# Kernel optimization log

Hardware: AMD Instinct MI355X
Metric: run time of the kernel (lower is better)

Reference implementation:

```python
import jax, jax.numpy as jnp
import numpy as np

N, E, D, H = 50000, 800000, 128, 8
HD = D // H
EPS = 1e-5


def _layernorm(x, w, b):
    # Custom LayerNorm from the repo: divides by (unbiased std + eps), not sqrt(var+eps)
    mu = x.mean(axis=-1, keepdims=True)
    sd = x.std(axis=-1, keepdims=True, ddof=1)
    return (x - mu) / (sd + EPS) * w + b


def setup_inputs() -> dict:
    key = jax.random.key(0)
    ks = jax.random.split(key, 16)
    s = 1.0 / np.sqrt(D)
    inp = {
        "feats": jax.random.normal(ks[0], (N, D), jnp.float32),
        "edge_index": jax.random.randint(ks[1], (E, 2), 0, N, jnp.int32),
        "Wq": jax.random.normal(ks[2], (D, D), jnp.float32) * s,
        "bq": jnp.zeros((D,), jnp.float32),
        "Wk": jax.random.normal(ks[3], (D, D), jnp.float32) * s,
        "bk": jnp.zeros((D,), jnp.float32),
        "Wv": jax.random.normal(ks[4], (D, D), jnp.float32) * s,
        "bv": jnp.zeros((D,), jnp.float32),
        "Wo": jax.random.normal(ks[5], (D, D), jnp.float32) * s,
        "bo": jnp.zeros((D,), jnp.float32),
        "ln1_w": jnp.ones((D,), jnp.float32),
        "ln1_b": jnp.zeros((D,), jnp.float32),
        "ln2_w": jnp.ones((D,), jnp.float32),
        "ln2_b": jnp.zeros((D,), jnp.float32),
        "W1": jax.random.normal(ks[6], (4 * D, D), jnp.float32) * s,
        "b1": jnp.zeros((4 * D,), jnp.float32),
        "W2": jax.random.normal(ks[7], (D, 4 * D), jnp.float32) * (1.0 / np.sqrt(4 * D)),
        "b2": jnp.zeros((D,), jnp.float32),
    }
    return inp


def reference(feats, edge_index, Wq, bq, Wk, bk, Wv, bv, Wo, bo,
              ln1_w, ln1_b, ln2_w, ln2_b, W1, b1, W2, b2):
    n = feats.shape[0]
    row, col = edge_index[:, 0], edge_index[:, 1]

    # --- multi-head dot-product attention over edges (dropout = identity, eval mode) ---
    x2 = _layernorm(feats, ln1_w, ln1_b)
    q = (x2 @ Wq.T + bq).reshape(n, H, HD)
    k = (x2 @ Wk.T + bk).reshape(n, H, HD)
    v = (x2 @ Wv.T + bv).reshape(n, H, HD)

    # per-edge scores: q[col] . k[row] / sqrt(head_dim)  -> [E, H]
    scores = jnp.einsum('ehd,ehd->eh', q[col], k[row]) / np.sqrt(HD).astype(np.float32)

    # scatter softmax normalized over groups of `row`
    smax = jax.ops.segment_max(scores, row, num_segments=n)       # [N, H]
    ex = jnp.exp(scores - smax[row])                              # [E, H]
    denom = jax.ops.segment_sum(ex, row, num_segments=n)         # [N, H]
    alpha = ex / denom[row]                                       # [E, H]

    # weighted messages, aggregated at col via scatter_add
    msg = alpha[:, :, None] * v[row]                              # [E, H, HD]
    agg = jax.ops.segment_sum(msg, col, num_segments=n).reshape(n, D)
    att = agg @ Wo.T + bo

    feats = feats + att  # residual 1

    # --- MLP block: note ReLU after BOTH linears (fc_dims=[4D, D], D != 1) ---
    x2 = _layernorm(feats, ln2_w, ln2_b)
    h = jax.nn.relu(x2 @ W1.T + b1)
    h = jax.nn.relu(h @ W2.T + b2)
    feats = feats + h  # residual 2
    return feats
```

## Files before the change

kernel.cpp:

```cpp
#include <hip/hip_runtime.h>
#include <hip/hip_bf16.h>
#include <math.h>

#define H_HEADS 8
constexpr float LN_EPS = 1e-5f;
constexpr int NBCH = 64;
constexpr int NSEG = 4;

using short8 = __attribute__((ext_vector_type(8))) short;
using f32x4  = __attribute__((ext_vector_type(4))) float;
using half2v = __attribute__((ext_vector_type(2))) _Float16;

#if defined(__has_builtin)
#  if __has_builtin(__builtin_amdgcn_fdot2)
#    define HAS_FDOT2 1
#  endif
#endif
#ifndef HAS_FDOT2
#  define HAS_FDOT2 0
#endif

__device__ __forceinline__ ushort f2bf(float v){
  __hip_bfloat16 h = __float2bfloat16(v);
  return *reinterpret_cast<ushort*>(&h);
}
__device__ __forceinline__ float bf2f(ushort u){
  return __uint_as_float(((unsigned)u) << 16);
}

__device__ __forceinline__ void stage16(const ushort* g, ushort* l){
  __builtin_amdgcn_global_load_lds((const __attribute__((address_space(1))) unsigned*)g,
                                   (__attribute__((address_space(3))) unsigned*)l,
                                   16, 0, 0);
}

__global__ void ln_kernel(const float* __restrict__ x, const float* __restrict__ w,
                          const float* __restrict__ b, ushort* __restrict__ out, int nrows){
  int wid = threadIdx.x >> 6, lane = threadIdx.x & 63;
  int r = blockIdx.x * (blockDim.x >> 6) + wid;
  if (r >= nrows) return;
  float2 v = ((const float2*)(x + (size_t)r*128))[lane];
  float s = v.x + v.y;
  #pragma unroll
  for (int o = 32; o; o >>= 1) s += __shfl_xor(s, o);
  float mu = s * (1.0f/128.0f);
  float d0 = v.x - mu, d1 = v.y - mu;
  float ss = d0*d0 + d1*d1;
  #pragma unroll
  for (int o = 32; o; o >>= 1) ss += __shfl_xor(ss, o);
  float sd = sqrtf(ss * (1.0f/127.0f));
  float inv = 1.0f / (sd + LN_EPS);
  float2 wv = ((const float2*)w)[lane];
  float2 bv = ((const float2*)b)[lane];
  ushort2 o2 = { f2bf(d0*inv*wv.x + bv.x), f2bf(d1*inv*wv.y + bv.y) };
  ((ushort2*)(out + (size_t)r*128))[lane] = o2;
}

struct CvtArgs { const float* s[6]; ushort* d[6]; int cnt[6]; };
__global__ void cvt6_kernel(CvtArgs a){
  int w = blockIdx.y;
  int i = blockIdx.x*blockDim.x + threadIdx.x;
  if (i < a.cnt[w]) a.d[w][i] = f2bf(a.s[w][i]);
}

template<int K, int RELU, int RESID, int OUTMODE>
__device__ __forceinline__ void gemm_lds_body(
    const ushort* __restrict__ A, const ushort* __restrict__ W,
    const float* __restrict__ bias, const float* __restrict__ resid,
    void* __restrict__ out, int M, int Nout, int cb, ushort* Wl){
  constexpr int NCH = K / 128;
  int t = threadIdx.x;
  int wid = t >> 6, lane = t & 63;
  int mb = blockIdx.x * 64 + wid * 16;
  int lrow = lane & 15, kgrp = lane >> 4;
  int row = mb + lrow;
  bool rowok = row < M;
  const ushort* arow = A + (size_t)(rowok ? row : (M-1)) * K + kgrp*8;

  f32x4 acc[8] = {};
  short8 af[2][4];

  #pragma unroll
  for (int p = 0; p < 8; ++p){
    int L = p*256 + t;
    int colp = L >> 4, sp = L & 15;
    stage16(W + (size_t)colp*K + ((sp ^ (colp & 7)) << 3),
            (ushort*)((char*)Wl + ((size_t)(p*256 + (t & ~63)))*16));
  }
  #pragma unroll
  for (int kk = 0; kk < 4; ++kk)
    af[0][kk] = *(const short8*)(arow + kk*32);

  #pragma unroll
  for (int ci = 0; ci < NCH; ++ci){
    __syncthreads();
    int cur = ci & 1;
    if (ci + 1 < NCH){
      #pragma unroll
      for (int kk = 0; kk < 4; ++kk)
        af[cur^1][kk] = *(const short8*)(arow + (ci+1)*128 + kk*32);
    }
    #pragma unroll
    for (int kk = 0; kk < 4; ++kk){
      #pragma unroll
      for (int nt = 0; nt < 8; ++nt){
        int colc = nt*16 + lrow;
        int g = kk*4 + kgrp;
        short8 bfv = *(const short8*)((const char*)Wl + colc*256 + ((g ^ (colc & 7))*16));
        acc[nt] = __builtin_amdgcn_mfma_f32_16x16x32_bf16(af[cur][kk], bfv, acc[nt], 0, 0, 0);
      }
    }
    if (ci + 1 < NCH){
      __syncthreads();
      const ushort* Wc = W + (ci+1)*128;
      #pragma unroll
      for (int p = 0; p < 8; ++p){
        int L = p*256 + t;
        int colp = L >> 4, sp = L & 15;
        stage16(Wc + (size_t)colp*K + ((sp ^ (colp & 7)) << 3),
                (ushort*)((char*)Wl + ((size_t)(p*256 + (t & ~63)))*16));
      }
    }
  }

  int r0 = mb + kgrp*4;
  #pragma unroll
  for (int nt = 0; nt < 8; ++nt){
    int c = cb + nt*16 + lrow;
    float bsum = bias[c];
    #pragma unroll
    for (int i = 0; i < 4; ++i){
      int r = r0 + i;
      if (r >= M) continue;
      float v = acc[nt][i] + bsum;
      if (RELU)  v = fmaxf(v, 0.0f);
      if (RESID) v += resid[(size_t)r*Nout + c];
      if (OUTMODE == 1) ((ushort*)out)[(size_t)r*Nout + c] = f2bf(v);
      else if (OUTMODE == 2){
        _Float16 hv = (_Float16)v;
        ((ushort*)out)[(size_t)r*Nout + c] = __builtin_bit_cast(ushort, hv);
      } else ((float*)out)[(size_t)r*Nout + c] = v;
    }
  }
}

template<int K, int RELU, int RESID, int OUTMODE>
__global__ __launch_bounds__(256) void gemm_lds(
    const ushort* __restrict__ A, const ushort* __restrict__ Wfull,
    const float* __restrict__ bias, const float* __restrict__ resid,
    void* __restrict__ out, int M, int Nout){
  __shared__ __align__(16) ushort Wl[16384];
  int cb = blockIdx.y * 128;
  gemm_lds_body<K,RELU,RESID,OUTMODE>(A, Wfull + (size_t)cb*K, bias, resid, out, M, Nout, cb, Wl);
}

__global__ __launch_bounds__(256) void qkv_lds(
    const ushort* __restrict__ A, const ushort* __restrict__ Wcat,
    const float* __restrict__ bq, const float* __restrict__ bk, const float* __restrict__ bv,
    ushort* __restrict__ qb, ushort* __restrict__ kb, ushort* __restrict__ vb, int M){
  __shared__ __align__(16) ushort Wl[16384];
  int y = blockIdx.y;
  const float* bias = (y==0) ? bq : (y==1) ? bk : bv;
  ushort* out = (y==0) ? qb : (y==1) ? kb : vb;
  if (y == 2)
    gemm_lds_body<128,0,0,1>(A, Wcat + (size_t)y*16384, bias, nullptr, out, M, 128, 0, Wl);
  else
    gemm_lds_body<128,0,0,2>(A, Wcat + (size_t)y*16384, bias, nullptr, out, M, 128, 0, Wl);
}

__global__ __launch_bounds__(256) void hist_seg2(const int* __restrict__ ei,
    unsigned* __restrict__ copies, int E, int n, int nw, int chunk, int nsb){
  __shared__ unsigned hh[12544];
  int b = blockIdx.x, s = blockIdx.y, t = threadIdx.x;
  int bin0 = s * nsb;
  int bin1 = min(bin0 + nsb, n);
  int words = (bin1 - bin0 + 1) >> 1;
  for (int i = t; i < 2*words; i += 256) hh[i] = 0;
  __syncthreads();
  int lo = b*chunk, hi = min(lo + chunk, E);
  for (int e = lo + t; e < hi; e += 256){
    int2 rc = ((const int2*)ei)[e];
    if (rc.x >= bin0 && rc.x < bin1)
      atomicAdd(&hh[(rc.x - bin0) >> 1], 1u << ((rc.x & 1)*16));
    if (rc.y >= bin0 && rc.y < bin1)
      atomicAdd(&hh[words + ((rc.y - bin0) >> 1)], 1u << ((rc.y & 1)*16));
  }
  __syncthreads();
  unsigned* d0 = copies + (size_t)b*nw + (bin0 >> 1);
  unsigned* d1 = copies + (size_t)(NBCH + b)*nw + (bin0 >> 1);
  for (int i = t; i < words; i += 256){ d0[i] = hh[i]; d1[i] = hh[words + i]; }
}

__global__ __launch_bounds__(256) void scan_fold(const unsigned* __restrict__ copies,
    int* __restrict__ cnt2, ushort* __restrict__ choff, int n, int nw){
  int y = blockIdx.y;
  int bin = blockIdx.x*256 + threadIdx.x;
  if (bin >= n) return;
  const unsigned* cp = copies + (size_t)y*NBCH*nw + (bin >> 1);
  int sh = (bin & 1)*16;
  int run = 0;
  for (int b = 0; b < NBCH; ++b){
    int c = (int)((cp[(size_t)b*nw] >> sh) & 0xffffu);
    choff[((size_t)y*NBCH + b)*n + bin] = (ushort)run;
    run += c;
  }
  cnt2[(size_t)y*n + bin] = run;
}

__global__ __launch_bounds__(256) void scan_reduce(const int* __restrict__ cnt0,
                                                   int* __restrict__ partial, int n, int nb){
  const int* cnt = cnt0 + (size_t)blockIdx.y * n;
  int t = threadIdx.x;
  int base = blockIdx.x*1024 + t*4;
  int s = 0;
  #pragma unroll
  for (int j = 0; j < 4; ++j){ int i = base+j; if (i < n) s += cnt[i]; }
  __shared__ int sm[256];
  sm[t] = s; __syncthreads();
  for (int off = 128; off; off >>= 1){
    if (t < off) sm[t] += sm[t+off];
    __syncthreads();
  }
  if (t == 0) partial[blockIdx.y*nb + blockIdx.x] = sm[0];
}

__global__ __launch_bounds__(256) void scan_mid(int* __restrict__ partial, int nb,
                                                int* __restrict__ rptr, int* __restrict__ cptr, int n){
  int y = blockIdx.y;
  int* p = partial + y*nb;
  int t = threadIdx.x;
  __shared__ int sm[256];
  sm[t] = (t < nb) ? p[t] : 0;
  __syncthreads();
  for (int off = 1; off < 256; off <<= 1){
    int v = (t >= off) ? sm[t-off] : 0;
    __syncthreads();
    sm[t] += v;
    __syncthreads();
  }
  if (t < nb) p[t] = (t == 0) ? 0 : sm[t-1];
  if (t == 0) (y ? cptr : rptr)[n] = sm[255];
}

__global__ __launch_bounds__(256) void scan_scatter(const int* __restrict__ cnt0,
                                                    const int* __restrict__ partial,
                                                    int* __restrict__ rptr, int* __restrict__ cptr,
                                                    int n, int nb){
  int y = blockIdx.y;
  const int* cnt = cnt0 + (size_t)y * n;
  int* ptr = y ? cptr : rptr;
  int t = threadIdx.x;
  int base = blockIdx.x*1024 + t*4;
  int v[4]; int s = 0;
  #pragma unroll
  for (int j = 0; j < 4; ++j){ int i = base+j; v[j] = (i<n)?cnt[i]:0; s += v[j]; }
  __shared__ int sm[256];
  sm[t] = s; __syncthreads();
  for (int off = 1; off < 256; off <<= 1){
    int x = (t >= off) ? sm[t-off] : 0;
    __syncthreads();
    sm[t] += x;
    __syncthreads();
  }
  int pre = partial[y*nb + blockIdx.x] + ((t==0)?0:sm[t-1]);
  #pragma unroll
  for (int j = 0; j < 4; ++j){
    int i = base+j;
    if (i < n){ ptr[i] = pre; pre += v[j]; }
  }
}

__global__ __launch_bounds__(256) void fill_r_seg(const int* __restrict__ ei,
    const int* __restrict__ rptr, const ushort* __restrict__ choffR,
    int* __restrict__ rcol, int* __restrict__ pose, int E, int n, int chunk, int nsb){
  __shared__ unsigned hh[8192];
  int b = blockIdx.x, s = blockIdx.y, t = threadIdx.x;
  int bin0 = s * nsb;
  int bin1 = min(bin0 + nsb, n);
  int words = (bin1 - bin0 + 1) >> 1;
  for (int i = t; i < words; i += 256) hh[i] = 0;
  __syncthreads();
  const ushort* chb = choffR + (size_t)b*n;
  int lo = b*chunk, hi = min(lo + chunk, E);
  for (int e = lo + t; e < hi; e += 256){
    int2 rc = ((const int2*)ei)[e];
    int bin = rc.x;
    if (bin < bin0 || bin >= bin1) continue;
    int sh = (bin & 1)*16;
    unsigned old = atomicAdd(&hh[(bin - bin0) >> 1], 1u << sh);
    int rank = (int)((old >> sh) & 0xffffu);
    int pos = rptr[bin] + (int)chb[bin] + rank;
    rcol[pos] = rc.y;
    pose[e] = pos;
  }
}

__global__ __launch_bounds__(256) void fill_c_seg(const int* __restrict__ ei,
    const int* __restrict__ cptr, const ushort* __restrict__ choffC,
    const int* __restrict__ pose, int* __restrict__ crow, int* __restrict__ cposr,
    int E, int n, int chunk, int nsb){
  __shared__ unsigned hh[8192];
  int b = blockIdx.x, s = blockIdx.y, t = threadIdx.x;
  int bin0 = s * nsb;
  int bin1 = min(bin0 + nsb, n);
  int words = (bin1 - bin0 + 1) >> 1;
  for (int i = t; i < words; i += 256) hh[i] = 0;
  __syncthreads();
  const ushort* chb = choffC + (size_t)b*n;
  int lo = b*chunk, hi = min(lo + chunk, E);
  for (int e = lo + t; e < hi; e += 256){
    int2 rc = ((const int2*)ei)[e];
    int bin = rc.y;
    if (bin < bin0 || bin >= bin1) continue;
    int sh = (bin & 1)*16;
    unsigned old = atomicAdd(&hh[(bin - bin0) >> 1], 1u << sh);
    int rank = (int)((old >> sh) & 0xffffu);
    int pos = cptr[bin] + (int)chb[bin] + rank;
    crow[pos] = rc.x;
    cposr[pose[e]] = pos;
  }
}

__device__ __forceinline__ float qdot16h(const ushort* __restrict__ qb, int c, int h,
                                         const half2v* kf2){
  const int4* qp = (const int4*)(qb + (size_t)c*128 + h*16);
  int4 a = qp[0], b = qp[1];
  int qa[8] = {a.x, a.y, a.z, a.w, b.x, b.y, b.z, b.w};
  float s = 0.f;
#if HAS_FDOT2
  #pragma unroll
  for (int i = 0; i < 8; ++i)
    s = __builtin_amdgcn_fdot2(__builtin_bit_cast(half2v, qa[i]), kf2[i], s, false);
#else
  #pragma unroll
  for (int i = 0; i < 8; ++i){
    half2v q2 = __builtin_bit_cast(half2v, qa[i]);
    s += (float)q2.x * (float)kf2[i].x + (float)q2.y * (float)kf2[i].y;
  }
#endif
  return s * 0.25f;
}

template<int NS>
__device__ __forceinline__ void softmax_rows(const ushort* __restrict__ qb,
    const int* __restrict__ rcol, const int* __restrict__ cposr,
    ushort* __restrict__ cbuf, const half2v* kf2, int lo, int hi, int h, int el){
  float sreg[NS];
  float m = -1e30f;
  #pragma unroll
  for (int ts = 0; ts < NS; ++ts){
    int j = lo + el + ts*8;
    float s = (j < hi) ? qdot16h(qb, rcol[j], h, kf2) : -1e30f;
    sreg[ts] = s;
    m = fmaxf(m, s);
  }
  if (NS == 8)
    for (int j = lo + el + 64; j < hi; j += 8)
      m = fmaxf(m, qdot16h(qb, rcol[j], h, kf2));
  #pragma unroll
  for (int o = 8; o < 64; o <<= 1) m = fmaxf(m, __shfl_xor(m, o));

  float d = 0.f;
  #pragma unroll
  for (int ts = 0; ts < NS; ++ts){
    int j = lo + el + ts*8;
    if (j < hi){ float e = __expf(sreg[ts] - m); sreg[ts] = e; d += e; }
  }
  if (NS == 8)
    for (int j = lo + el + 64; j < hi; j += 8)
      d += __expf(qdot16h(qb, rcol[j], h, kf2) - m);
  #pragma unroll
  for (int o = 8; o < 64; o <<= 1) d += __shfl_xor(d, o);
  float invd = 1.0f / d;

  #pragma unroll
  for (int ts = 0; ts < NS; ++ts){
    int j = lo + el + ts*8;
    if (j < hi) cbuf[(size_t)cposr[j]*8 + h] = f2bf(sreg[ts] * invd);
  }
  if (NS == 8)
    for (int j = lo + el + 64; j < hi; j += 8){
      float s = qdot16h(qb, rcol[j], h, kf2);
      cbuf[(size_t)cposr[j]*8 + h] = f2bf(__expf(s - m) * invd);
    }
}

__global__ void row_softmax_kernel(const ushort* __restrict__ qb, const ushort* __restrict__ kb,
                                   const int* __restrict__ rptr, const int* __restrict__ rcol,
                                   const int* __restrict__ cposr,
                                   ushort* __restrict__ cbuf, int n){
  int wid = threadIdx.x >> 6, lane = threadIdx.x & 63;
  int r = blockIdx.x * (blockDim.x >> 6) + wid;
  if (r >= n) return;
  int lo = rptr[r], hi = rptr[r+1];
  if (lo >= hi) return;
  int h = lane & 7, el = lane >> 3;

  half2v kf2[8];
  {
    const int4* kp = (const int4*)(kb + (size_t)r*128 + h*16);
    int4 k0 = kp[0], k1 = kp[1];
    kf2[0] = __builtin_bit_cast(half2v, k0.x);
    kf2[1] = __builtin_bit_cast(half2v, k0.y);
    kf2[2] = __builtin_bit_cast(half2v, k0.z);
    kf2[3] = __builtin_bit_cast(half2v, k0.w);
    kf2[4] = __builtin_bit_cast(half2v, k1.x);
    kf2[5] = __builtin_bit_cast(half2v, k1.y);
    kf2[6] = __builtin_bit_cast(half2v, k1.z);
    kf2[7] = __builtin_bit_cast(half2v, k1.w);
  }

  int deg = hi - lo;
  if (deg <= 16)      softmax_rows<2>(qb, rcol, cposr, cbuf, kf2, lo, hi, h, el);
  else if (deg <= 32) softmax_rows<4>(qb, rcol, cposr, cbuf, kf2, lo, hi, h, el);
  else                softmax_rows<8>(qb, rcol, cposr, cbuf, kf2, lo, hi, h, el);
}

__global__ void agg_kernel(const ushort* __restrict__ vb, const ushort* __restrict__ cbuf,
                           const int* __restrict__ cptr, const int* __restrict__ crow,
                           ushort* __restrict__ aggb, int n){
  int wid = threadIdx.x >> 6, lane = threadIdx.x & 63;
  int node = blockIdx.x * (blockDim.x >> 6) + wid;
  if (node >= n) return;
  int lo = cptr[node], hi = cptr[node+1];
  int oct = lane >> 3, l8 = lane & 7;
  float acc[16] = {};
  for (int j = lo + oct; j < hi; j += 8){
    float a = bf2f(cbuf[(size_t)j*8 + l8]);
    int row = crow[j];
    const short8* vp = (const short8*)(vb + (size_t)row*128 + l8*16);
    short8 v0 = vp[0], v1 = vp[1];
    #pragma unroll
    for (int i = 0; i < 8; ++i){
      acc[i]   = fmaf(a, bf2f((ushort)v0[i]), acc[i]);
      acc[8+i] = fmaf(a, bf2f((ushort)v1[i]), acc[8+i]);
    }
  }
  #pragma unroll
  for (int i = 0; i < 16; ++i){
    acc[i] += __shfl_xor(acc[i], 8);
    acc[i] += __shfl_xor(acc[i], 16);
    acc[i] += __shfl_xor(acc[i], 32);
  }
  if (oct == 0){
    short8 o0, o1;
    #pragma unroll
    for (int i = 0; i < 8; ++i){ o0[i] = (short)f2bf(acc[i]); o1[i] = (short)f2bf(acc[8+i]); }
    short8* op = (short8*)(aggb + (size_t)node*128 + l8*16);
    op[0] = o0; op[1] = o1;
  }
}

extern "C" void kernel_launch(void* const* d_in, const int* in_sizes, int n_in,
                              void* d_out, int out_size, void* d_ws, size_t ws_size,
                              hipStream_t stream){
  const float* feats = (const float*)d_in[0];
  const int*   ei    = (const int*)  d_in[1];
  const float* Wq = (const float*)d_in[2];
  const float* bq = (const float*)d_in[3];
  const float* Wk = (const float*)d_in[4];
  const float* bk = (const float*)d_in[5];
  const float* Wv = (const float*)d_in[6];
  const float* bv = (const float*)d_in[7];
  const float* Wo = (const float*)d_in[8];
  const float* bo = (const float*)d_in[9];
  const float* ln1w = (const float*)d_in[10];
  const float* ln1b = (const float*)d_in[11];
  const float* ln2w = (const float*)d_in[12];
  const float* ln2b = (const float*)d_in[13];
  const float* W1 = (const float*)d_in[14];
  const float* b1 = (const float*)d_in[15];
  const float* W2 = (const float*)d_in[16];
  const float* b2 = (const float*)d_in[17];
  float* outp = (float*)d_out;

  int n = in_sizes[0] / 128;
  int E = in_sizes[1] / 2;
  int nw = (n + 1) >> 1;
  int chunk = (E + NBCH - 1) / NBCH;
  int nsb = (((n + NSEG - 1) / NSEG) + 1) & ~1;

  const size_t ND  = (size_t)n * 128;
  const size_t ND2 = ND / 2;
  const size_t EH  = (size_t)E * H_HEADS;

  float* ws = (float*)d_ws;
  ushort* x2b  = (ushort*)ws;
  ushort* qb   = (ushort*)(ws + ND2);
  ushort* kb   = (ushort*)(ws + 2*ND2);
  ushort* vb   = (ushort*)(ws + 3*ND2);
  ushort* cbuf = (ushort*)(ws + 4*ND2);
  ushort* aggb = (ushort*)(ws + 4*ND2 + EH/2);
  int* crow    = (int*)(ws + 5*ND2 + EH/2);
  int* cposr   = crow + E;
  int* rcol    = cposr + E;
  int* pose    = rcol + E;
  int* rptr    = pose + E;
  int* cptr    = rptr + (n + 4);
  int* cnt2    = cptr + (n + 4);
  ushort* choff = (ushort*)(cnt2 + 2*n);
  unsigned* copies = (unsigned*)(choff + (size_t)2*NBCH*n);
  int* partial = (int*)(copies + (size_t)2*NBCH*nw);
  ushort* wbuf = (ushort*)(partial + 512);
  ushort* Wqb = wbuf;
  ushort* Wkb = Wqb + 16384;
  ushort* Wvb = Wkb + 16384;
  ushort* Wob = Wvb + 16384;
  ushort* W1b = Wob + 16384;
  ushort* W2b = W1b + 65536;
  ushort* h1  = qb;

  CvtArgs ca;
  ca.s[0]=Wq; ca.s[1]=Wk; ca.s[2]=Wv; ca.s[3]=Wo; ca.s[4]=W1; ca.s[5]=W2;
  ca.d[0]=Wqb; ca.d[1]=Wkb; ca.d[2]=Wvb; ca.d[3]=Wob; ca.d[4]=W1b; ca.d[5]=W2b;
  ca.cnt[0]=ca.cnt[1]=ca.cnt[2]=ca.cnt[3]=16384; ca.cnt[4]=ca.cnt[5]=65536;
  cvt6_kernel<<<dim3(65536/256, 6), 256, 0, stream>>>(ca);

  int nb = (n + 1023)/1024;
  hist_seg2 <<<dim3(NBCH,NSEG), 256, 0, stream>>>(ei, copies, E, n, nw, chunk, nsb);
  scan_fold <<<dim3((n+255)/256,2), 256, 0, stream>>>(copies, cnt2, choff, n, nw);
  scan_reduce <<<dim3(nb,2), 256, 0, stream>>>(cnt2, partial, n, nb);
  scan_mid    <<<dim3(1,2),  256, 0, stream>>>(partial, nb, rptr, cptr, n);
  scan_scatter<<<dim3(nb,2), 256, 0, stream>>>(cnt2, partial, rptr, cptr, n, nb);
  fill_r_seg<<<dim3(NBCH,NSEG), 256, 0, stream>>>(ei, rptr, choff,                  rcol, pose, E, n, chunk, nsb);
  fill_c_seg<<<dim3(NBCH,NSEG), 256, 0, stream>>>(ei, cptr, choff + (size_t)NBCH*n, pose, crow, cposr, E, n, chunk, nsb);

  ln_kernel<<<(n+3)/4, 256, 0, stream>>>(feats, ln1w, ln1b, x2b, n);

  int gm = (n + 63)/64;
  qkv_lds<<<dim3(gm,3), 256, 0, stream>>>(x2b, Wqb, bq, bk, bv, qb, kb, vb, n);

  row_softmax_kernel<<<(n+3)/4, 256, 0, stream>>>(qb, kb, rptr, rcol, cposr, cbuf, n);

  agg_kernel<<<(n+3)/4, 256, 0, stream>>>(vb, cbuf, cptr, crow, aggb, n);

  gemm_lds<128,0,1,0><<<dim3(gm,1), 256, 0, stream>>>(aggb, Wob, bo, feats, outp, n, 128);

  ln_kernel<<<(n+3)/4, 256, 0, stream>>>(outp, ln2w, ln2b, x2b, n);

  gemm_lds<128,1,0,1><<<dim3(gm,4), 256, 0, stream>>>(x2b, W1b, b1, nullptr, h1,  n, 512);
  gemm_lds<512,1,1,0><<<dim3(gm,1), 256, 0, stream>>>(h1,  W2b, b2, outp,    outp, n, 128);
}
```

Measured before the change: 305.2 us.

## Fuse Wo GEMM with residual and LayerNorm2; use 128-row 512-thread GEMM blocks

Adds a gemm_wo_ln2 kernel that computes the output projection, adds bias and the residual, then applies LayerNorm2 in registers and writes the bf16 x2b buffer directly. This removes the separate ln_kernel launch and one fp32 read of outp. All GEMM blocks now cover 128 rows with 512 threads, so each block stages the weight tile once for twice as many rows. Waves past M skip loads and compute but still reach the barriers. The larger blocks mean fewer blocks in total and possibly lower occupancy.

```diff
diff --git a/kernel.cpp b/kernel.cpp
--- a/kernel.cpp
+++ b/kernel.cpp
@@ -71,9 +71,10 @@
   constexpr int NCH = K / 128;
   int t = threadIdx.x;
   int wid = t >> 6, lane = t & 63;
-  int mb = blockIdx.x * 64 + wid * 16;
+  int mb = blockIdx.x * 128 + wid * 16;
   int lrow = lane & 15, kgrp = lane >> 4;
   int row = mb + lrow;
+  bool waveok = mb < M;
   bool rowok = row < M;
   const ushort* arow = A + (size_t)(rowok ? row : (M-1)) * K + kgrp*8;
 
@@ -81,47 +82,52 @@
   short8 af[2][4];
 
   #pragma unroll
-  for (int p = 0; p < 8; ++p){
-    int L = p*256 + t;
+  for (int p = 0; p < 4; ++p){
+    int L = p*512 + t;
     int colp = L >> 4, sp = L & 15;
     stage16(W + (size_t)colp*K + ((sp ^ (colp & 7)) << 3),
-            (ushort*)((char*)Wl + ((size_t)(p*256 + (t & ~63)))*16));
-  }
-  #pragma unroll
-  for (int kk = 0; kk < 4; ++kk)
-    af[0][kk] = *(const short8*)(arow + kk*32);
+            (ushort*)((char*)Wl + ((size_t)(p*512 + (t & ~63)))*16));
+  }
+  if (waveok){
+    #pragma unroll
+    for (int kk = 0; kk < 4; ++kk)
+      af[0][kk] = *(const short8*)(arow + kk*32);
+  }
 
   #pragma unroll
   for (int ci = 0; ci < NCH; ++ci){
     __syncthreads();
     int cur = ci & 1;
-    if (ci + 1 < NCH){
+    if (waveok){
+      if (ci + 1 < NCH){
+        #pragma unroll
+        for (int kk = 0; kk < 4; ++kk)
+          af[cur^1][kk] = *(const short8*)(arow + (ci+1)*128 + kk*32);
+      }
       #pragma unroll
-      for (int kk = 0; kk < 4; ++kk)
-        af[cur^1][kk] = *(const short8*)(arow + (ci+1)*128 + kk*32);
-    }
-    #pragma unroll
-    for (int kk = 0; kk < 4; ++kk){
-      #pragma unroll
-      for (int nt = 0; nt < 8; ++nt){
-        int colc = nt*16 + lrow;
-        int g = kk*4 + kgrp;
-        short8 bfv = *(const short8*)((const char*)Wl + colc*256 + ((g ^ (colc & 7))*16));
-        acc[nt] = __builtin_amdgcn_mfma_f32_16x16x32_bf16(af[cur][kk], bfv, acc[nt], 0, 0, 0);
+      for (int kk = 0; kk < 4; ++kk){
+        #pragma unroll
+        for (int nt = 0; nt < 8; ++nt){
+          int colc = nt*16 + lrow;
+          int g = kk*4 + kgrp;
+          short8 bfv = *(const short8*)((const char*)Wl + colc*256 + ((g ^ (colc & 7))*16));
+          acc[nt] = __builtin_amdgcn_mfma_f32_16x16x32_bf16(af[cur][kk], bfv, acc[nt], 0, 0, 0);
+        }
       }
     }
     if (ci + 1 < NCH){
       __syncthreads();
       const ushort* Wc = W + (ci+1)*128;
       #pragma unroll
-      for (int p = 0; p < 8; ++p){
-        int L = p*256 + t;
+      for (int p = 0; p < 4; ++p){
+        int L = p*512 + t;
         int colp = L >> 4, sp = L & 15;
         stage16(Wc + (size_t)colp*K + ((sp ^ (colp & 7)) << 3),
-                (ushort*)((char*)Wl + ((size_t)(p*256 + (t & ~63)))*16));
+                (ushort*)((char*)Wl + ((size_t)(p*512 + (t & ~63)))*16));
       }
     }
   }
+  if (!waveok) return;
 
   int r0 = mb + kgrp*4;
   #pragma unroll
@@ -145,7 +151,7 @@
 }
 
 template<int K, int RELU, int RESID, int OUTMODE>
-__global__ __launch_bounds__(256) void gemm_lds(
+__global__ __launch_bounds__(512) void gemm_lds(
     const ushort* __restrict__ A, const ushort* __restrict__ Wfull,
     const float* __restrict__ bias, const float* __restrict__ resid,
     void* __restrict__ out, int M, int Nout){
@@ -154,7 +160,7 @@
   gemm_lds_body<K,RELU,RESID,OUTMODE>(A, Wfull + (size_t)cb*K, bias, resid, out, M, Nout, cb, Wl);
 }
 
-__global__ __launch_bounds__(256) void qkv_lds(
+__global__ __launch_bounds__(512) void qkv_lds(
     const ushort* __restrict__ A, const ushort* __restrict__ Wcat,
     const float* __restrict__ bq, const float* __restrict__ bk, const float* __restrict__ bv,
     ushort* __restrict__ qb, ushort* __restrict__ kb, ushort* __restrict__ vb, int M){
@@ -166,6 +172,97 @@
     gemm_lds_body<128,0,0,1>(A, Wcat + (size_t)y*16384, bias, nullptr, out, M, 128, 0, Wl);
   else
     gemm_lds_body<128,0,0,2>(A, Wcat + (size_t)y*16384, bias, nullptr, out, M, 128, 0, Wl);
+}
+
+__global__ __launch_bounds__(512) void gemm_wo_ln2(
+    const ushort* __restrict__ A, const ushort* __restrict__ W,
+    const float* __restrict__ bias, const float* __restrict__ feats,
+    const float* __restrict__ lnw, const float* __restrict__ lnb,
+    float* __restrict__ outp, ushort* __restrict__ x2b, int M){
+  constexpr int K = 128;
+  __shared__ __align__(16) ushort Wl[16384];
+  int t = threadIdx.x;
+  int wid = t >> 6, lane = t & 63;
+  int mb = blockIdx.x * 128 + wid * 16;
+  int lrow = lane & 15, kgrp = lane >> 4;
+  int row = mb + lrow;
+  bool waveok = mb < M;
+  bool rowok = row < M;
+  const ushort* arow = A + (size_t)(rowok ? row : (M-1)) * K + kgrp*8;
+
+  f32x4 acc[8] = {};
+  short8 af[4];
+
+  #pragma unroll
+  for (int p = 0; p < 4; ++p){
+    int L = p*512 + t;
+    int colp = L >> 4, sp = L & 15;
+    stage16(W + (size_t)colp*K + ((sp ^ (colp & 7)) << 3),
+            (ushort*)((char*)Wl + ((size_t)(p*512 + (t & ~63)))*16));
+  }
+  if (waveok){
+    #pragma unroll
+    for (int kk = 0; kk < 4; ++kk)
+      af[kk] = *(const short8*)(arow + kk*32);
+  }
+  __syncthreads();
+  if (!waveok) return;
+
+  #pragma unroll
+  for (int kk = 0; kk < 4; ++kk){
+    #pragma unroll
+    for (int nt = 0; nt < 8; ++nt){
+      int colc = nt*16 + lrow;
+      int g = kk*4 + kgrp;
+      short8 bfv = *(const short8*)((const char*)Wl + colc*256 + ((g ^ (colc & 7))*16));
+      acc[nt] = __builtin_amdgcn_mfma_f32_16x16x32_bf16(af[kk], bfv, acc[nt], 0, 0, 0);
+    }
+  }
+
+  int r0 = mb + kgrp*4;
+  float vv[8][4];
+  float lw[8], lb[8];
+  #pragma unroll
+  for (int nt = 0; nt < 8; ++nt){
+    int c = nt*16 + lrow;
+    float bsum = bias[c];
+    lw[nt] = lnw[c]; lb[nt] = lnb[c];
+    #pragma unroll
+    for (int i = 0; i < 4; ++i){
+      int r = r0 + i;
+      float v = 0.f;
+      if (r < M){
+        v = acc[nt][i] + bsum + feats[(size_t)r*128 + c];
+        outp[(size_t)r*128 + c] = v;
+      }
+      vv[nt][i] = v;
+    }
+  }
+  #pragma unroll
+  for (int i = 0; i < 4; ++i){
+    int r = r0 + i;
+    float s = 0.f;
+    #pragma unroll
+    for (int nt = 0; nt < 8; ++nt) s += vv[nt][i];
+    #pragma unroll
+    for (int o = 1; o < 16; o <<= 1) s += __shfl_xor(s, o);
+    float mu = s * (1.0f/128.0f);
+    float ss = 0.f;
+    float d[8];
+    #pragma unroll
+    for (int nt = 0; nt < 8; ++nt){ d[nt] = vv[nt][i] - mu; ss += d[nt]*d[nt]; }
+    #pragma unroll
+    for (int o = 1; o < 16; o <<= 1) ss += __shfl_xor(ss, o);
+    float sd = sqrtf(ss * (1.0f/127.0f));
+    float inv = 1.0f / (sd + LN_EPS);
+    if (r < M){
+      #pragma unroll
+      for (int nt = 0; nt < 8; ++nt){
+        int c = nt*16 + lrow;
+        x2b[(size_t)r*128 + c] = f2bf(d[nt]*inv*lw[nt] + lb[nt]);
+      }
+    }
+  }
 }
 
 __global__ __launch_bounds__(256) void hist_seg2(const int* __restrict__ ei,
@@ -527,17 +624,15 @@
 
   ln_kernel<<<(n+3)/4, 256, 0, stream>>>(feats, ln1w, ln1b, x2b, n);
 
-  int gm = (n + 63)/64;
-  qkv_lds<<<dim3(gm,3), 256, 0, stream>>>(x2b, Wqb, bq, bk, bv, qb, kb, vb, n);
+  int gm = (n + 127)/128;
+  qkv_lds<<<dim3(gm,3), 512, 0, stream>>>(x2b, Wqb, bq, bk, bv, qb, kb, vb, n);
 
   row_softmax_kernel<<<(n+3)/4, 256, 0, stream>>>(qb, kb, rptr, rcol, cposr, cbuf, n);
 
   agg_kernel<<<(n+3)/4, 256, 0, stream>>>(vb, cbuf, cptr, crow, aggb, n);
 
-  gemm_lds<128,0,1,0><<<dim3(gm,1), 256, 0, stream>>>(aggb, Wob, bo, feats, outp, n, 128);
-
-  ln_kernel<<<(n+3)/4, 256, 0, stream>>>(outp, ln2w, ln2b, x2b, n);
-
-  gemm_lds<128,1,0,1><<<dim3(gm,4), 256, 0, stream>>>(x2b, W1b, b1, nullptr, h1,  n, 512);
-  gemm_lds<512,1,1,0><<<dim3(gm,1), 256, 0, stream>>>(h1,  W2b, b2, outp,    outp, n, 128);
-}
+  gemm_wo_ln2<<<gm, 512, 0, stream>>>(aggb, Wob, bo, feats, ln2w, ln2b, outp, x2b, n);
+
+  gemm_lds<128,1,0,1><<<dim3(gm,4), 512, 0, stream>>>(x2b, W1b, b1, nullptr, h1,  n, 512);
+  gemm_lds<512,1,1,0><<<dim3(gm,1), 512, 0, stream>>>(h1,  W2b, b2, outp,    outp, n, 128);
+}
```

After: 284.3 us. -6.9%, faster.
